# Kernel tuning notes

Measured on AMD Instinct MI355X. Metric: run time of the kernel, lower is better.

Reference implementation:

```python
import jax, jax.numpy as jnp
import numpy as np

L, D, N = 4096, 1024, 16  # seq_len, d_model, hiddens_per_input


def setup_inputs() -> dict:
    key = jax.random.key(0)
    ks = jax.random.split(key, 9)
    x = jax.random.normal(ks[0], (L, D), dtype=jnp.float32)
    # Delta param (pre-softplus); softplus(Delta) > 0 is the discretization step
    Delta = jax.random.normal(ks[1], (D,), dtype=jnp.float32)
    # A stored as (re, im); default scheme uses A_re = -1 (stable), theta in [0, 2pi)
    A_re = -(0.5 + 0.5 * jax.random.uniform(ks[2], (D, N), dtype=jnp.float32))
    A_im = jax.random.uniform(ks[3], (D, N), dtype=jnp.float32) * 2.0 * jnp.pi
    scale = 1.0 / jnp.sqrt(jnp.float32(D))  # matrix_init: randn / sqrt(shape[0])
    B_re = jax.random.normal(ks[4], (D, N), dtype=jnp.float32) * scale
    B_im = jax.random.normal(ks[5], (D, N), dtype=jnp.float32) * scale
    C_re = jax.random.normal(ks[6], (D, N), dtype=jnp.float32) * scale
    C_im = jax.random.normal(ks[7], (D, N), dtype=jnp.float32) * scale
    D_param = jax.random.normal(ks[8], (D,), dtype=jnp.float32) * scale
    return {"x": x, "Delta": Delta, "A_re": A_re, "A_im": A_im,
            "B_re": B_re, "B_im": B_im, "C_re": C_re, "C_im": C_im,
            "D_param": D_param}


def _binary_operator_diag(q_i, q_j):
    """Associative op for diagonal linear recurrence h_j = A_j h_{j-1} + b_j."""
    A_i, b_i = q_i
    A_j, b_j = q_j
    return (A_j * A_i, A_j * b_i + b_j)


def reference(x, Delta, A_re, A_im, B_re, B_im, C_re, C_im, D_param):
    Bc = B_re + 1j * B_im                      # (D, N) complex
    Cc = C_re + 1j * C_im                      # (D, N) complex
    Ac = A_re + 1j * A_im                      # (D, N) complex
    dt = jax.nn.softplus(Delta)                # (D,)
    # shared_Delta=True branch: Lambda = exp(dt[:, None] * A), repeated over L
    Lam = jnp.exp(dt[:, None] * Ac)            # (D, N) complex
    Lambda_elements = jnp.broadcast_to(Lam[None, :, :], (x.shape[0], *Lam.shape))
    # Bu = einsum('D, D N, L D -> L D N', dt, B, x)
    Bu_elements = jnp.einsum('D,DN,LD->LDN', dt.astype(Bc.dtype), Bc,
                             x.astype(Bc.dtype))
    _, hidden_states = jax.lax.associative_scan(
        _binary_operator_diag, (Lambda_elements, Bu_elements))  # (L, D, N)
    out = jnp.einsum('LDN,DN->LD', hidden_states, Cc) + D_param[None, :] * x
    return out.real
```

## Files before the change

### kernel.cpp

```cpp
#include <hip/hip_runtime.h>
#include <math.h>

constexpr int L  = 4096;
constexpr int D  = 1024;
constexpr int N  = 16;
constexpr int NC = 64;
constexpr int T  = L / NC;
constexpr int DG = 64;
constexpr int G  = D / DG;

__device__ __forceinline__ float softplus_f(float v) {
    return fmaxf(v, 0.0f) + log1pf(expf(-fabsf(v)));
}

__device__ __forceinline__ void lam_fast(float ar, float ai, float dt,
                                         float& lr, float& li) {
    float e = __expf(ar * dt);
    float s, c;
    __sincosf(ai * dt, &s, &c);
    lr = e * c;
    li = e * s;
}

__global__ __launch_bounds__(256, 4) void k_local(
    const float* __restrict__ x,
    const float* __restrict__ Delta,
    const float* __restrict__ A_re, const float* __restrict__ A_im,
    float2* __restrict__ s2)
{
    __shared__ float xs[T * DG];
    const int c  = blockIdx.x >> 4;
    const int dg = blockIdx.x & 15;
    const int t  = threadIdx.x;

    const float* xg = x + (size_t)c * T * D + dg * DG;
    #pragma unroll
    for (int it = 0; it < 4; ++it) {
        int f = t * 4 + it * 1024;
        int row = f >> 6, col = f & 63;
        *(float4*)&xs[row * DG + col] =
            *(const float4*)(xg + (size_t)row * D + col);
    }

    const int q = t & 3, dl = t >> 2;
    const int d = dg * DG + dl;
    const float dt = softplus_f(Delta[d]);
    float Lr[4], Li[4];
    {
        float4 a0 = *(const float4*)(A_re + d * N + q * 4);
        float4 a1 = *(const float4*)(A_im + d * N + q * 4);
        const float ar[4] = {a0.x, a0.y, a0.z, a0.w};
        const float ai[4] = {a1.x, a1.y, a1.z, a1.w};
        #pragma unroll
        for (int j = 0; j < 4; ++j) lam_fast(ar[j], ai[j], dt, Lr[j], Li[j]);
    }
    __syncthreads();

    float gr[4] = {0, 0, 0, 0}, gi[4] = {0, 0, 0, 0};
    #pragma unroll
    for (int i = 0; i < T; ++i) {
        float xv = xs[i * DG + dl];
        #pragma unroll
        for (int j = 0; j < 4; ++j) {
            float t2 = fmaf(-Li[j], gi[j], xv);
            float nr = fmaf(Lr[j], gr[j], t2);
            gi[j] = fmaf(Lr[j], gi[j], Li[j] * gr[j]);
            gr[j] = nr;
        }
    }
    #pragma unroll
    for (int j = 0; j < 4; ++j)
        s2[((size_t)c * N + q * 4 + j) * D + d] = make_float2(gr[j], gi[j]);
}

__global__ __launch_bounds__(256) void k_scan(
    const float* __restrict__ Delta,
    const float* __restrict__ A_re, const float* __restrict__ A_im,
    float2* __restrict__ s2)
{
    const int tid = blockIdx.x * 256 + threadIdx.x;
    const int d = tid & (D - 1);
    const int n = tid >> 10;

    const float dt = softplus_f(Delta[d]);
    float Lr, Li;
    lam_fast(A_re[d * N + n], A_im[d * N + n], dt, Lr, Li);
    #pragma unroll
    for (int k = 0; k < 6; ++k) {
        float nr = Lr * Lr - Li * Li;
        Li = 2.0f * Lr * Li;
        Lr = nr;
    }

    float cr = 0.0f, ci = 0.0f;
    #pragma unroll
    for (int c0 = 0; c0 < NC; c0 += 16) {
        float2 sv[16];
        #pragma unroll
        for (int u = 0; u < 16; ++u)
            sv[u] = s2[(size_t)(c0 + u) * (N * D) + tid];
        #pragma unroll
        for (int u = 0; u < 16; ++u) {
            s2[(size_t)(c0 + u) * (N * D) + tid] = make_float2(cr, ci);
            float nr = fmaf(Lr, cr, fmaf(-Li, ci, sv[u].x));
            ci = fmaf(Lr, ci, fmaf(Li, cr, sv[u].y));
            cr = nr;
        }
    }
}

__global__ __launch_bounds__(256, 4) void k_out(
    const float* __restrict__ x,
    const float* __restrict__ Delta,
    const float* __restrict__ A_re, const float* __restrict__ A_im,
    const float* __restrict__ B_re, const float* __restrict__ B_im,
    const float* __restrict__ C_re, const float* __restrict__ C_im,
    const float* __restrict__ Dp,
    const float2* __restrict__ s2,
    float* __restrict__ out)
{
    __shared__ float xs[T * DG];
    const int c  = blockIdx.x >> 4;
    const int dg = blockIdx.x & 15;
    const int t  = threadIdx.x;

    const float* xg = x + (size_t)c * T * D + dg * DG;
    #pragma unroll
    for (int it = 0; it < 4; ++it) {
        int f = t * 4 + it * 1024;
        int row = f >> 6, col = f & 63;
        *(float4*)&xs[row * DG + col] =
            *(const float4*)(xg + (size_t)row * D + col);
    }

    const int q = t & 3, dl = t >> 2;
    const int d = dg * DG + dl;
    const float dt  = softplus_f(Delta[d]);
    const float dpv = Dp[d];

    float Lr[4], Li[4], Cr[4], Ci[4], gr[4], gi[4];
    {
        const int pidx = d * N + q * 4;
        float4 a0 = *(const float4*)(A_re + pidx);
        float4 a1 = *(const float4*)(A_im + pidx);
        float4 b0 = *(const float4*)(B_re + pidx);
        float4 b1 = *(const float4*)(B_im + pidx);
        float4 c0 = *(const float4*)(C_re + pidx);
        float4 c1 = *(const float4*)(C_im + pidx);
        const float ar[4] = {a0.x, a0.y, a0.z, a0.w};
        const float ai[4] = {a1.x, a1.y, a1.z, a1.w};
        const float br[4] = {b0.x, b0.y, b0.z, b0.w};
        const float bi[4] = {b1.x, b1.y, b1.z, b1.w};
        const float crr[4] = {c0.x, c0.y, c0.z, c0.w};
        const float cii[4] = {c1.x, c1.y, c1.z, c1.w};
        #pragma unroll
        for (int j = 0; j < 4; ++j) {
            lam_fast(ar[j], ai[j], dt, Lr[j], Li[j]);
            Cr[j] = dt * (crr[j] * br[j] - cii[j] * bi[j]);
            Ci[j] = dt * (crr[j] * bi[j] + cii[j] * br[j]);
        }
    }
    #pragma unroll
    for (int j = 0; j < 4; ++j) {
        float2 cv = s2[((size_t)c * N + q * 4 + j) * D + d];
        gr[j] = cv.x; gi[j] = cv.y;
    }
    float* og = out + (size_t)c * T * D + dg * DG;
    __syncthreads();

    #pragma unroll
    for (int ib = 0; ib < T / 4; ++ib) {
        float keep = 0.0f;
        #pragma unroll
        for (int u = 0; u < 4; ++u) {
            int i = ib * 4 + u;
            float xv = xs[i * DG + dl];
            float acc = 0.0f;
            #pragma unroll
            for (int j = 0; j < 4; ++j) {
                float t2 = fmaf(-Li[j], gi[j], xv);
                float nr = fmaf(Lr[j], gr[j], t2);
                gi[j] = fmaf(Lr[j], gi[j], Li[j] * gr[j]);
                gr[j] = nr;
                acc = fmaf(Cr[j], gr[j], acc);
                acc = fmaf(-Ci[j], gi[j], acc);
            }
            acc += __shfl_xor(acc, 1);
            acc += __shfl_xor(acc, 2);
            acc = fmaf(dpv, xv, acc);
            keep = (q == u) ? acc : keep;
        }
        og[(size_t)(ib * 4 + q) * D + dl] = keep;
    }
}

extern "C" void kernel_launch(void* const* d_in, const int* in_sizes, int n_in,
                              void* d_out, int out_size, void* d_ws, size_t ws_size,
                              hipStream_t stream) {
    const float* x     = (const float*)d_in[0];
    const float* Delta = (const float*)d_in[1];
    const float* A_re  = (const float*)d_in[2];
    const float* A_im  = (const float*)d_in[3];
    const float* B_re  = (const float*)d_in[4];
    const float* B_im  = (const float*)d_in[5];
    const float* C_re  = (const float*)d_in[6];
    const float* C_im  = (const float*)d_in[7];
    const float* Dp    = (const float*)d_in[8];
    float* out = (float*)d_out;
    float2* s2 = (float2*)d_ws;

    k_local<<<NC * G, 256, 0, stream>>>(x, Delta, A_re, A_im, s2);
    k_scan<<<(N * D) / 256, 256, 0, stream>>>(Delta, A_re, A_im, s2);
    k_out<<<NC * G, 256, 0, stream>>>(x, Delta, A_re, A_im, B_re, B_im,
                                      C_re, C_im, Dp, s2, out);
}
```

Measured before the change: 111.3 us.

## Fuse chunked scan into one kernel with per-block channel pairs and shared-memory carries

Replaces the three-kernel chunked scan (local sums, global carry scan, output pass) with a single kernel where each block owns two channels across the full sequence. Chunk sums and the cross-chunk carry scan live in shared memory, so the workspace round trip and two extra launches go away, and x is read only once. The cost is a serial carry scan on only 32 threads inside each block, and each thread now holds 8 states, which raises register pressure. The grid also shrinks to 512 blocks, and x loads become strided 8-byte reads per row, which may hurt coalescing.

```diff
diff --git a/kernel.cpp b/kernel.cpp
--- a/kernel.cpp
+++ b/kernel.cpp
@@ -1,13 +1,13 @@
 #include <hip/hip_runtime.h>
 #include <math.h>
 
-constexpr int L  = 4096;
-constexpr int D  = 1024;
-constexpr int N  = 16;
-constexpr int NC = 64;
-constexpr int T  = L / NC;
-constexpr int DG = 64;
-constexpr int G  = D / DG;
+constexpr int L   = 4096;
+constexpr int D   = 1024;
+constexpr int N   = 16;
+constexpr int CPB = 2;
+constexpr int NB  = D / CPB;
+constexpr int NCB = 64;
+constexpr int T   = L / NCB;
 
 __device__ __forceinline__ float softplus_f(float v) {
     return fmaxf(v, 0.0f) + log1pf(expf(-fabsf(v)));
@@ -22,162 +22,144 @@
     li = e * s;
 }
 
-__global__ __launch_bounds__(256, 4) void k_local(
+__global__ __launch_bounds__(256, 2) void k_fused(
     const float* __restrict__ x,
     const float* __restrict__ Delta,
     const float* __restrict__ A_re, const float* __restrict__ A_im,
-    float2* __restrict__ s2)
+    const float* __restrict__ B_re, const float* __restrict__ B_im,
+    const float* __restrict__ C_re, const float* __restrict__ C_im,
+    const float* __restrict__ Dp,
+    float* __restrict__ out)
 {
-    __shared__ float xs[T * DG];
-    const int c  = blockIdx.x >> 4;
-    const int dg = blockIdx.x & 15;
+    __shared__ float  xs[T * 128];
+    __shared__ float2 sums[NCB * 32];
+
+    const int b  = blockIdx.x;
+    const int d0 = (b & 7) * 128 + (b >> 3) * 2;
     const int t  = threadIdx.x;
 
-    const float* xg = x + (size_t)c * T * D + dg * DG;
-    #pragma unroll
-    for (int it = 0; it < 4; ++it) {
-        int f = t * 4 + it * 1024;
-        int row = f >> 6, col = f & 63;
-        *(float4*)&xs[row * DG + col] =
-            *(const float4*)(xg + (size_t)row * D + col);
+    {
+        const int sct = t & 63;
+        const int si  = t >> 6;
+        float2 v[16];
+        #pragma unroll
+        for (int k = 0; k < 16; ++k) {
+            int l = sct * T + si * 16 + k;
+            v[k] = *(const float2*)(x + (size_t)l * D + d0);
+        }
+        #pragma unroll
+        for (int k = 0; k < 16; ++k) {
+            int i = si * 16 + k;
+            *(float2*)&xs[i * 128 + sct * 2] = v[k];
+        }
     }
 
-    const int q = t & 3, dl = t >> 2;
-    const int d = dg * DG + dl;
+    const int h  = t & 1;
+    const int dd = (t >> 1) & 1;
+    const int ct = t >> 2;
+    const int d  = d0 + dd;
     const float dt = softplus_f(Delta[d]);
-    float Lr[4], Li[4];
+
+    float Lr[8], Li[8];
     {
-        float4 a0 = *(const float4*)(A_re + d * N + q * 4);
-        float4 a1 = *(const float4*)(A_im + d * N + q * 4);
-        const float ar[4] = {a0.x, a0.y, a0.z, a0.w};
-        const float ai[4] = {a1.x, a1.y, a1.z, a1.w};
+        const int base = d * N + h * 8;
+        float4 a0 = *(const float4*)(A_re + base);
+        float4 a1 = *(const float4*)(A_re + base + 4);
+        float4 m0 = *(const float4*)(A_im + base);
+        float4 m1 = *(const float4*)(A_im + base + 4);
+        const float ar[8] = {a0.x, a0.y, a0.z, a0.w, a1.x, a1.y, a1.z, a1.w};
+        const float ai[8] = {m0.x, m0.y, m0.z, m0.w, m1.x, m1.y, m1.z, m1.w};
         #pragma unroll
-        for (int j = 0; j < 4; ++j) lam_fast(ar[j], ai[j], dt, Lr[j], Li[j]);
+        for (int j = 0; j < 8; ++j) lam_fast(ar[j], ai[j], dt, Lr[j], Li[j]);
     }
     __syncthreads();
 
-    float gr[4] = {0, 0, 0, 0}, gi[4] = {0, 0, 0, 0};
-    #pragma unroll
+    float gr[8] = {0, 0, 0, 0, 0, 0, 0, 0}, gi[8] = {0, 0, 0, 0, 0, 0, 0, 0};
+    #pragma unroll 8
     for (int i = 0; i < T; ++i) {
-        float xv = xs[i * DG + dl];
+        float xv = xs[i * 128 + ct * 2 + dd];
         #pragma unroll
-        for (int j = 0; j < 4; ++j) {
+        for (int j = 0; j < 8; ++j) {
             float t2 = fmaf(-Li[j], gi[j], xv);
             float nr = fmaf(Lr[j], gr[j], t2);
             gi[j] = fmaf(Lr[j], gi[j], Li[j] * gr[j]);
             gr[j] = nr;
         }
     }
-    #pragma unroll
-    for (int j = 0; j < 4; ++j)
-        s2[((size_t)c * N + q * 4 + j) * D + d] = make_float2(gr[j], gi[j]);
-}
+    {
+        float2* sp = &sums[ct * 32 + dd * 16 + h * 8];
+        #pragma unroll
+        for (int j = 0; j < 8; ++j) sp[j] = make_float2(gr[j], gi[j]);
+    }
+    __syncthreads();
 
-__global__ __launch_bounds__(256) void k_scan(
-    const float* __restrict__ Delta,
-    const float* __restrict__ A_re, const float* __restrict__ A_im,
-    float2* __restrict__ s2)
-{
-    const int tid = blockIdx.x * 256 + threadIdx.x;
-    const int d = tid & (D - 1);
-    const int n = tid >> 10;
-
-    const float dt = softplus_f(Delta[d]);
-    float Lr, Li;
-    lam_fast(A_re[d * N + n], A_im[d * N + n], dt, Lr, Li);
-    #pragma unroll
-    for (int k = 0; k < 6; ++k) {
-        float nr = Lr * Lr - Li * Li;
-        Li = 2.0f * Lr * Li;
-        Lr = nr;
+    if (t < 32) {
+        const int dd2 = t >> 4, n2 = t & 15;
+        const int d2  = d0 + dd2;
+        const float dt2 = softplus_f(Delta[d2]);
+        float lr, li;
+        lam_fast(A_re[d2 * N + n2], A_im[d2 * N + n2], dt2, lr, li);
+        #pragma unroll
+        for (int k = 0; k < 6; ++k) {
+            float nr = lr * lr - li * li;
+            li = 2.0f * lr * li;
+            lr = nr;
+        }
+        float cr = 0.0f, ci = 0.0f;
+        #pragma unroll
+        for (int c0 = 0; c0 < NCB; c0 += 16) {
+            float2 sv[16];
+            #pragma unroll
+            for (int u = 0; u < 16; ++u) sv[u] = sums[(c0 + u) * 32 + t];
+            #pragma unroll
+            for (int u = 0; u < 16; ++u) {
+                sums[(c0 + u) * 32 + t] = make_float2(cr, ci);
+                float nr = fmaf(lr, cr, fmaf(-li, ci, sv[u].x));
+                ci = fmaf(lr, ci, fmaf(li, cr, sv[u].y));
+                cr = nr;
+            }
+        }
     }
 
-    float cr = 0.0f, ci = 0.0f;
-    #pragma unroll
-    for (int c0 = 0; c0 < NC; c0 += 16) {
-        float2 sv[16];
+    float Cr[8], Ci[8];
+    {
+        const int base = d * N + h * 8;
+        float4 b0 = *(const float4*)(B_re + base);
+        float4 b1 = *(const float4*)(B_re + base + 4);
+        float4 e0 = *(const float4*)(B_im + base);
+        float4 e1 = *(const float4*)(B_im + base + 4);
+        float4 f0 = *(const float4*)(C_re + base);
+        float4 f1 = *(const float4*)(C_re + base + 4);
+        float4 g0 = *(const float4*)(C_im + base);
+        float4 g1 = *(const float4*)(C_im + base + 4);
+        const float br[8] = {b0.x, b0.y, b0.z, b0.w, b1.x, b1.y, b1.z, b1.w};
+        const float bi[8] = {e0.x, e0.y, e0.z, e0.w, e1.x, e1.y, e1.z, e1.w};
+        const float cr[8] = {f0.x, f0.y, f0.z, f0.w, f1.x, f1.y, f1.z, f1.w};
+        const float ci[8] = {g0.x, g0.y, g0.z, g0.w, g1.x, g1.y, g1.z, g1.w};
         #pragma unroll
-        for (int u = 0; u < 16; ++u)
-            sv[u] = s2[(size_t)(c0 + u) * (N * D) + tid];
-        #pragma unroll
-        for (int u = 0; u < 16; ++u) {
-            s2[(size_t)(c0 + u) * (N * D) + tid] = make_float2(cr, ci);
-            float nr = fmaf(Lr, cr, fmaf(-Li, ci, sv[u].x));
-            ci = fmaf(Lr, ci, fmaf(Li, cr, sv[u].y));
-            cr = nr;
+        for (int j = 0; j < 8; ++j) {
+            Cr[j] = dt * (cr[j] * br[j] - ci[j] * bi[j]);
+            Ci[j] = dt * (cr[j] * bi[j] + ci[j] * br[j]);
         }
     }
-}
-
-__global__ __launch_bounds__(256, 4) void k_out(
-    const float* __restrict__ x,
-    const float* __restrict__ Delta,
-    const float* __restrict__ A_re, const float* __restrict__ A_im,
-    const float* __restrict__ B_re, const float* __restrict__ B_im,
-    const float* __restrict__ C_re, const float* __restrict__ C_im,
-    const float* __restrict__ Dp,
-    const float2* __restrict__ s2,
-    float* __restrict__ out)
-{
-    __shared__ float xs[T * DG];
-    const int c  = blockIdx.x >> 4;
-    const int dg = blockIdx.x & 15;
-    const int t  = threadIdx.x;
-
-    const float* xg = x + (size_t)c * T * D + dg * DG;
-    #pragma unroll
-    for (int it = 0; it < 4; ++it) {
-        int f = t * 4 + it * 1024;
-        int row = f >> 6, col = f & 63;
-        *(float4*)&xs[row * DG + col] =
-            *(const float4*)(xg + (size_t)row * D + col);
-    }
-
-    const int q = t & 3, dl = t >> 2;
-    const int d = dg * DG + dl;
-    const float dt  = softplus_f(Delta[d]);
     const float dpv = Dp[d];
-
-    float Lr[4], Li[4], Cr[4], Ci[4], gr[4], gi[4];
-    {
-        const int pidx = d * N + q * 4;
-        float4 a0 = *(const float4*)(A_re + pidx);
-        float4 a1 = *(const float4*)(A_im + pidx);
-        float4 b0 = *(const float4*)(B_re + pidx);
-        float4 b1 = *(const float4*)(B_im + pidx);
-        float4 c0 = *(const float4*)(C_re + pidx);
-        float4 c1 = *(const float4*)(C_im + pidx);
-        const float ar[4] = {a0.x, a0.y, a0.z, a0.w};
-        const float ai[4] = {a1.x, a1.y, a1.z, a1.w};
-        const float br[4] = {b0.x, b0.y, b0.z, b0.w};
-        const float bi[4] = {b1.x, b1.y, b1.z, b1.w};
-        const float crr[4] = {c0.x, c0.y, c0.z, c0.w};
-        const float cii[4] = {c1.x, c1.y, c1.z, c1.w};
-        #pragma unroll
-        for (int j = 0; j < 4; ++j) {
-            lam_fast(ar[j], ai[j], dt, Lr[j], Li[j]);
-            Cr[j] = dt * (crr[j] * br[j] - cii[j] * bi[j]);
-            Ci[j] = dt * (crr[j] * bi[j] + cii[j] * br[j]);
-        }
-    }
-    #pragma unroll
-    for (int j = 0; j < 4; ++j) {
-        float2 cv = s2[((size_t)c * N + q * 4 + j) * D + d];
-        gr[j] = cv.x; gi[j] = cv.y;
-    }
-    float* og = out + (size_t)c * T * D + dg * DG;
     __syncthreads();
 
-    #pragma unroll
-    for (int ib = 0; ib < T / 4; ++ib) {
+    {
+        const float2* cp = &sums[ct * 32 + dd * 16 + h * 8];
+        #pragma unroll
+        for (int j = 0; j < 8; ++j) { gr[j] = cp[j].x; gi[j] = cp[j].y; }
+    }
+    #pragma unroll 4
+    for (int ib = 0; ib < T / 2; ++ib) {
         float keep = 0.0f;
         #pragma unroll
-        for (int u = 0; u < 4; ++u) {
-            int i = ib * 4 + u;
-            float xv = xs[i * DG + dl];
+        for (int u = 0; u < 2; ++u) {
+            int i = ib * 2 + u;
+            float xv = xs[i * 128 + ct * 2 + dd];
             float acc = 0.0f;
             #pragma unroll
-            for (int j = 0; j < 4; ++j) {
+            for (int j = 0; j < 8; ++j) {
                 float t2 = fmaf(-Li[j], gi[j], xv);
                 float nr = fmaf(Lr[j], gr[j], t2);
                 gi[j] = fmaf(Lr[j], gi[j], Li[j] * gr[j]);
@@ -186,11 +168,10 @@
                 acc = fmaf(-Ci[j], gi[j], acc);
             }
             acc += __shfl_xor(acc, 1);
-            acc += __shfl_xor(acc, 2);
             acc = fmaf(dpv, xv, acc);
-            keep = (q == u) ? acc : keep;
+            keep = (h == u) ? acc : keep;
         }
-        og[(size_t)(ib * 4 + q) * D + dl] = keep;
+        out[(size_t)(ct * T + ib * 2 + h) * D + d] = keep;
     }
 }
 
@@ -207,10 +188,7 @@
     const float* C_im  = (const float*)d_in[7];
     const float* Dp    = (const float*)d_in[8];
     float* out = (float*)d_out;
-    float2* s2 = (float2*)d_ws;
 
-    k_local<<<NC * G, 256, 0, stream>>>(x, Delta, A_re, A_im, s2);
-    k_scan<<<(N * D) / 256, 256, 0, stream>>>(Delta, A_re, A_im, s2);
-    k_out<<<NC * G, 256, 0, stream>>>(x, Delta, A_re, A_im, B_re, B_im,
-                                      C_re, C_im, Dp, s2, out);
+    k_fused<<<NB, 256, 0, stream>>>(x, Delta, A_re, A_im, B_re, B_im,
+                                    C_re, C_im, Dp, out);
 }
```

Measured after the change: 106.9 us. 3.9% less time.
